# Kernel optimization log

Hardware: AMD Instinct MI355X
Metric: run time of the kernel (lower is better)

The kernel has to match this reference:

```python
import jax, jax.numpy as jnp
import numpy as np

EMBED_DIM = 1024
NUM_HEADS = 16
HEAD_DIM = EMBED_DIM // NUM_HEADS
SCALE = HEAD_DIM ** -0.5
EPS = 1e-5


def layer_norm(x, gamma, beta):
    mu = jnp.mean(x, axis=-1, keepdims=True)
    var = jnp.var(x, axis=-1, keepdims=True)
    return (x - mu) * jax.lax.rsqrt(var + EPS) * gamma + beta


def setup_inputs() -> dict:
    key = jax.random.key(0)
    ks = jax.random.split(key, 12)
    d = EMBED_DIM
    xav = (6.0 / (d + d)) ** 0.5
    x = jax.random.normal(ks[0], (4, 1024, d), dtype=jnp.float32)
    Wq = jax.random.uniform(ks[1], (d, d), jnp.float32, -xav, xav)
    Wk = jax.random.uniform(ks[2], (d, d), jnp.float32, -xav, xav)
    Wv = jax.random.uniform(ks[3], (d, d), jnp.float32, -xav, xav)
    Wo = jax.random.uniform(ks[4], (d, d), jnp.float32, -xav, xav)
    bq = jnp.zeros((d,), jnp.float32)
    bk = jnp.zeros((d,), jnp.float32)
    bv = jnp.zeros((d,), jnp.float32)
    bo = jnp.zeros((d,), jnp.float32)
    ones = jnp.ones((d,), jnp.float32)
    zeros = jnp.zeros((d,), jnp.float32)
    return {
        "x": x,
        "Wq": Wq, "bq": bq, "Wk": Wk, "bk": bk, "Wv": Wv, "bv": bv,
        "Wo": Wo, "bo": bo,
        "qn_g": ones, "qn_b": zeros,
        "kn_g": ones, "kn_b": zeros,
        "vn_g": ones, "vn_b": zeros,
        "on_g": ones, "on_b": zeros,
    }


def reference(x, Wq, bq, Wk, bk, Wv, bv, Wo, bo,
              qn_g, qn_b, kn_g, kn_b, vn_g, vn_b, on_g, on_b):
    B, S, D = x.shape
    H, Hd = NUM_HEADS, HEAD_DIM
    # projections (nn.Linear: x @ W.T + b) followed by LayerNorm
    Q = layer_norm(x @ Wq.T + bq, qn_g, qn_b) * SCALE
    K = layer_norm(x @ Wk.T + bk, kn_g, kn_b)
    V = layer_norm(x @ Wv.T + bv, vn_g, vn_b)
    Q = Q.reshape(B, S, H, Hd).transpose(0, 2, 1, 3)  # [B,H,S,Hd]
    K = K.reshape(B, S, H, Hd).transpose(0, 2, 1, 3)
    V = V.reshape(B, S, H, Hd).transpose(0, 2, 1, 3)
    scores = jnp.einsum('bhqd,bhkd->bhqk', Q, K)
    scores = jnp.clip(scores, -10.0, 10.0)
    attn = jax.nn.softmax(scores, axis=-1)  # dropout = identity at eval
    out = jnp.einsum('bhqk,bhkd->bhqd', attn, V)
    out = out.transpose(0, 2, 1, 3).reshape(B, S, D)
    out = out @ Wo.T + bo
    return layer_norm(out, on_g, on_b)
```

## Files before the change

kernel.cpp:

```cpp
#include <hip/hip_runtime.h>
#include <stdint.h>
#include <stddef.h>

typedef unsigned short u16;
typedef __bf16 bf16x8 __attribute__((ext_vector_type(8)));
typedef float f32x4 __attribute__((ext_vector_type(4)));
typedef u16 u16x8 __attribute__((ext_vector_type(8)));

#define SEQ    1024
#define DEMB   1024
#define MROWS  4096
#define NHEAD  16
#define HD     64
#define QSCALE 0.125f
#define LN_EPS 1e-5f

static __device__ __forceinline__ u16 f2bf(float f) {
  union { float f; unsigned u; } c; c.f = f;
  unsigned r = c.u + 0x7FFFu + ((c.u >> 16) & 1u);
  return (u16)(r >> 16);
}
static __device__ __forceinline__ float bf2f(unsigned h) {
  union { unsigned u; float f; } c; c.u = h << 16; return c.f;
}

static __device__ __forceinline__ void gload16(const void* g, void* l) {
  __builtin_amdgcn_global_load_lds((const __attribute__((address_space(1))) void*)g,
                                   (__attribute__((address_space(3))) void*)l, 16, 0, 0);
}

__global__ void cvt_kernel(const float* __restrict__ x,
                           const float* __restrict__ wq, const float* __restrict__ wk,
                           const float* __restrict__ wv, const float* __restrict__ wo,
                           u16* __restrict__ xb, u16* __restrict__ wb) {
  size_t e = ((size_t)blockIdx.x * blockDim.x + threadIdx.x) * 8;
  const float* src; u16* dst; size_t off;
  if (e < (size_t)MROWS * DEMB) { src = x; dst = xb; off = e; }
  else {
    size_t we = e - (size_t)MROWS * DEMB;
    int plane = (int)(we >> 20);
    src = (plane == 0) ? wq : (plane == 1) ? wk : (plane == 2) ? wv : wo;
    dst = wb + ((size_t)plane << 20);
    off = we & ((1u << 20) - 1);
  }
  float4 a = *(const float4*)(src + off);
  float4 b = *(const float4*)(src + off + 4);
  u16 o[8] = { f2bf(a.x), f2bf(a.y), f2bf(a.z), f2bf(a.w),
               f2bf(b.x), f2bf(b.y), f2bf(b.z), f2bf(b.w) };
  uint4 pk;
  pk.x = (unsigned)o[0] | ((unsigned)o[1] << 16);
  pk.y = (unsigned)o[2] | ((unsigned)o[3] << 16);
  pk.z = (unsigned)o[4] | ((unsigned)o[5] << 16);
  pk.w = (unsigned)o[6] | ((unsigned)o[7] << 16);
  *(uint4*)(dst + off) = pk;
}

__global__ __launch_bounds__(256)
void gemm_bt(const u16* __restrict__ A, const u16* __restrict__ B0,
             const u16* __restrict__ B1, const u16* __restrict__ B2,
             u16* __restrict__ C, int M, int N, int K) {
  __shared__ u16 lA[128 * 32];
  __shared__ u16 lB[128 * 32];
  const u16* Bp = (blockIdx.z == 0) ? B0 : (blockIdx.z == 1) ? B1 : B2;
  u16* Cp = C + (size_t)blockIdx.z * ((size_t)M * N);
  const int tid = threadIdx.x;
  const int w = tid >> 6, l = tid & 63;
  const int lr = l & 15, lg = l >> 4;
  const int m0 = blockIdx.x * 128, n0 = blockIdx.y * 128;
  const int wm = (w & 1) * 64, wn = (w >> 1) * 64;
  f32x4 acc[4][4] = {};
  const int cid0 = w * 64 + l;
  const int cid1 = 256 + w * 64 + l;
  const int rowA0 = cid0 >> 2, kc0 = (cid0 & 3) * 8;
  const int rowA1 = cid1 >> 2, kc1 = (cid1 & 3) * 8;
  for (int kt = 0; kt < K; kt += 32) {
    __syncthreads();
    gload16(A  + (size_t)(m0 + rowA0) * K + kt + kc0, lA + (size_t)(w * 64) * 8);
    gload16(A  + (size_t)(m0 + rowA1) * K + kt + kc1, lA + (size_t)(256 + w * 64) * 8);
    gload16(Bp + (size_t)(n0 + rowA0) * K + kt + kc0, lB + (size_t)(w * 64) * 8);
    gload16(Bp + (size_t)(n0 + rowA1) * K + kt + kc1, lB + (size_t)(256 + w * 64) * 8);
    __syncthreads();
    bf16x8 af[4], bfg[4];
#pragma unroll
    for (int mb = 0; mb < 4; ++mb)
      af[mb] = *(const bf16x8*)(lA + (wm + mb * 16 + lr) * 32 + lg * 8);
#pragma unroll
    for (int nb = 0; nb < 4; ++nb)
      bfg[nb] = *(const bf16x8*)(lB + (wn + nb * 16 + lr) * 32 + lg * 8);
#pragma unroll
    for (int mb = 0; mb < 4; ++mb)
#pragma unroll
      for (int nb = 0; nb < 4; ++nb)
        acc[mb][nb] = __builtin_amdgcn_mfma_f32_16x16x32_bf16(af[mb], bfg[nb], acc[mb][nb], 0, 0, 0);
  }
#pragma unroll
  for (int mb = 0; mb < 4; ++mb)
#pragma unroll
    for (int nb = 0; nb < 4; ++nb)
#pragma unroll
      for (int r = 0; r < 4; ++r) {
        int row = m0 + wm + mb * 16 + lg * 4 + r;
        int col = n0 + wn + nb * 16 + lr;
        Cp[(size_t)row * N + col] = f2bf(acc[mb][nb][r]);
      }
}

static __device__ __forceinline__ void block_reduce2(float& s1, float& s2, float* red) {
#pragma unroll
  for (int o = 32; o > 0; o >>= 1) { s1 += __shfl_xor(s1, o); s2 += __shfl_xor(s2, o); }
  int w = threadIdx.x >> 6, l = threadIdx.x & 63;
  if (l == 0) { red[w * 2] = s1; red[w * 2 + 1] = s2; }
  __syncthreads();
  s1 = red[0] + red[2] + red[4] + red[6];
  s2 = red[1] + red[3] + red[5] + red[7];
}

__global__ void ln_qkv_kernel(const u16* __restrict__ projb,
                              const float* __restrict__ bq, const float* __restrict__ bk,
                              const float* __restrict__ bv,
                              const float* __restrict__ qg, const float* __restrict__ qb,
                              const float* __restrict__ kg, const float* __restrict__ kb,
                              const float* __restrict__ vg, const float* __restrict__ vb,
                              u16* __restrict__ Qh, u16* __restrict__ Kh, u16* __restrict__ Vh) {
  __shared__ float red[8];
  const int row = blockIdx.x & (MROWS - 1);
  const int plane = blockIdx.x >> 12;
  const float* bias; const float* gam; const float* bet; u16* op; float scl;
  if (plane == 0)      { bias = bq; gam = qg; bet = qb; op = Qh; scl = QSCALE; }
  else if (plane == 1) { bias = bk; gam = kg; bet = kb; op = Kh; scl = 1.f; }
  else                 { bias = bv; gam = vg; bet = vb; op = Vh; scl = 1.f; }
  const u16* src = projb + ((size_t)plane * MROWS + row) * DEMB;
  const int t = threadIdx.x;
  uint2 pv = *(const uint2*)(src + t * 4);
  float4 v;
  v.x = bf2f(pv.x & 0xffffu); v.y = bf2f(pv.x >> 16);
  v.z = bf2f(pv.y & 0xffffu); v.w = bf2f(pv.y >> 16);
  float4 bz = *(const float4*)(bias + t * 4);
  v.x += bz.x; v.y += bz.y; v.z += bz.z; v.w += bz.w;
  float s1 = v.x + v.y + v.z + v.w;
  float s2 = v.x * v.x + v.y * v.y + v.z * v.z + v.w * v.w;
  block_reduce2(s1, s2, red);
  const float mean = s1 * (1.f / DEMB);
  const float var = s2 * (1.f / DEMB) - mean * mean;
  const float rstd = rsqrtf(var + LN_EPS);
  float4 gg = *(const float4*)(gam + t * 4);
  float4 bb = *(const float4*)(bet + t * 4);
  u16 o0 = f2bf(((v.x - mean) * rstd * gg.x + bb.x) * scl);
  u16 o1 = f2bf(((v.y - mean) * rstd * gg.y + bb.y) * scl);
  u16 o2 = f2bf(((v.z - mean) * rstd * gg.z + bb.z) * scl);
  u16 o3 = f2bf(((v.w - mean) * rstd * gg.w + bb.w) * scl);
  const int b = row >> 10, s = row & (SEQ - 1);
  const int h = t >> 4;
  u16* dst = op + ((size_t)(b * NHEAD + h) * SEQ + s) * HD + (t & 15) * 4;
  uint2 pk;
  pk.x = (unsigned)o0 | ((unsigned)o1 << 16);
  pk.y = (unsigned)o2 | ((unsigned)o3 << 16);
  *(uint2*)dst = pk;
}

__global__ __launch_bounds__(256)
void attn_kernel(const u16* __restrict__ Qh, const u16* __restrict__ Kh,
                 const u16* __restrict__ Vh, u16* __restrict__ AO) {
  __shared__ u16 Vt[64][72];
  __shared__ u16 Pt[4][16][72];
  const int qt = blockIdx.x & 15, bh = blockIdx.x >> 4;
  const int b = bh >> 4, h = bh & 15;
  const u16* Qp = Qh + (size_t)bh * SEQ * HD;
  const u16* Kp = Kh + (size_t)bh * SEQ * HD;
  const u16* Vp = Vh + (size_t)bh * SEQ * HD;
  const int tid = threadIdx.x, w = tid >> 6, l = tid & 63;
  const int lr = l & 15, lg = l >> 4;
  const int qrow = qt * 64 + w * 16 + lr;
  bf16x8 qa0 = *(const bf16x8*)(Qp + (size_t)qrow * HD + lg * 8);
  bf16x8 qa1 = *(const bf16x8*)(Qp + (size_t)qrow * HD + 32 + lg * 8);
  f32x4 o[4] = {};
  float rs[4] = {0.f, 0.f, 0.f, 0.f};
  for (int kt = 0; kt < SEQ / 64; ++kt) {
    __syncthreads();
#pragma unroll
    for (int i = 0; i < 2; ++i) {
      const int dc = w * 2 + i;
      u16x8 vv = *(const u16x8*)(Vp + (size_t)(kt * 64 + l) * HD + dc * 8);
#pragma unroll
      for (int ee = 0; ee < 8; ++ee) Vt[dc * 8 + ee][l] = vv[ee];
    }
#pragma unroll
    for (int kb = 0; kb < 4; ++kb) {
      const u16* kr = Kp + (size_t)(kt * 64 + kb * 16 + lr) * HD + lg * 8;
      bf16x8 k0 = *(const bf16x8*)kr;
      bf16x8 k1 = *(const bf16x8*)(kr + 32);
      f32x4 sv = {};
      sv = __builtin_amdgcn_mfma_f32_16x16x32_bf16(qa0, k0, sv, 0, 0, 0);
      sv = __builtin_amdgcn_mfma_f32_16x16x32_bf16(qa1, k1, sv, 0, 0, 0);
#pragma unroll
      for (int r = 0; r < 4; ++r) {
        float xx = fminf(10.f, fmaxf(-10.f, sv[r]));
        float p = exp2f(xx * 1.4426950408889634f);
        rs[r] += p;
        Pt[w][lg * 4 + r][kb * 16 + lr] = f2bf(p);
      }
    }
    __syncthreads();
    bf16x8 pa0 = *(const bf16x8*)(&Pt[w][lr][lg * 8]);
    bf16x8 pa1 = *(const bf16x8*)(&Pt[w][lr][32 + lg * 8]);
#pragma unroll
    for (int nb = 0; nb < 4; ++nb) {
      bf16x8 v0 = *(const bf16x8*)(&Vt[nb * 16 + lr][lg * 8]);
      bf16x8 v1 = *(const bf16x8*)(&Vt[nb * 16 + lr][32 + lg * 8]);
      o[nb] = __builtin_amdgcn_mfma_f32_16x16x32_bf16(pa0, v0, o[nb], 0, 0, 0);
      o[nb] = __builtin_amdgcn_mfma_f32_16x16x32_bf16(pa1, v1, o[nb], 0, 0, 0);
    }
  }
#pragma unroll
  for (int r = 0; r < 4; ++r) {
    float vsum = rs[r];
    vsum += __shfl_xor(vsum, 1);
    vsum += __shfl_xor(vsum, 2);
    vsum += __shfl_xor(vsum, 4);
    vsum += __shfl_xor(vsum, 8);
    rs[r] = vsum;
  }
#pragma unroll
  for (int nb = 0; nb < 4; ++nb)
#pragma unroll
    for (int r = 0; r < 4; ++r) {
      const int srow = qt * 64 + w * 16 + lg * 4 + r;
      const int col = h * HD + nb * 16 + lr;
      AO[((size_t)b * SEQ + srow) * DEMB + col] = f2bf(o[nb][r] / rs[r]);
    }
}

__global__ void ln_out_kernel(const u16* __restrict__ src0, const float* __restrict__ bo,
                              const float* __restrict__ og, const float* __restrict__ ob,
                              float* __restrict__ out) {
  __shared__ float red[8];
  const int row = blockIdx.x;
  const u16* src = src0 + (size_t)row * DEMB;
  const int t = threadIdx.x;
  uint2 pv = *(const uint2*)(src + t * 4);
  float4 v;
  v.x = bf2f(pv.x & 0xffffu); v.y = bf2f(pv.x >> 16);
  v.z = bf2f(pv.y & 0xffffu); v.w = bf2f(pv.y >> 16);
  float4 bz = *(const float4*)(bo + t * 4);
  v.x += bz.x; v.y += bz.y; v.z += bz.z; v.w += bz.w;
  float s1 = v.x + v.y + v.z + v.w;
  float s2 = v.x * v.x + v.y * v.y + v.z * v.z + v.w * v.w;
  block_reduce2(s1, s2, red);
  const float mean = s1 * (1.f / DEMB);
  const float var = s2 * (1.f / DEMB) - mean * mean;
  const float rstd = rsqrtf(var + LN_EPS);
  float4 gg = *(const float4*)(og + t * 4);
  float4 bb = *(const float4*)(ob + t * 4);
  float4 r;
  r.x = (v.x - mean) * rstd * gg.x + bb.x;
  r.y = (v.y - mean) * rstd * gg.y + bb.y;
  r.z = (v.z - mean) * rstd * gg.z + bb.z;
  r.w = (v.w - mean) * rstd * gg.w + bb.w;
  *(float4*)(out + (size_t)row * DEMB + t * 4) = r;
}

extern "C" void kernel_launch(void* const* d_in, const int* in_sizes, int n_in,
                              void* d_out, int out_size, void* d_ws, size_t ws_size,
                              hipStream_t stream) {
  (void)in_sizes; (void)n_in; (void)out_size; (void)ws_size;
  const float* x  = (const float*)d_in[0];
  const float* Wq = (const float*)d_in[1];
  const float* bq = (const float*)d_in[2];
  const float* Wk = (const float*)d_in[3];
  const float* bk = (const float*)d_in[4];
  const float* Wv = (const float*)d_in[5];
  const float* bv = (const float*)d_in[6];
  const float* Wo = (const float*)d_in[7];
  const float* bo = (const float*)d_in[8];
  const float* qg = (const float*)d_in[9];
  const float* qb = (const float*)d_in[10];
  const float* kg = (const float*)d_in[11];
  const float* kb = (const float*)d_in[12];
  const float* vg = (const float*)d_in[13];
  const float* vb = (const float*)d_in[14];
  const float* og = (const float*)d_in[15];
  const float* ob = (const float*)d_in[16];

  char* ws = (char*)d_ws;
  u16* xb    = (u16*)(ws);
  u16* wb    = (u16*)(ws + ((size_t)8  << 20));
  u16* projb = (u16*)(ws + ((size_t)16 << 20));
  u16* Qh    = (u16*)(ws + ((size_t)40 << 20));
  u16* Kh    = (u16*)(ws + ((size_t)48 << 20));
  u16* Vh    = (u16*)(ws + ((size_t)56 << 20));
  u16* AOp   = xb;
  u16* oprojb = projb;

  cvt_kernel<<<4096, 256, 0, stream>>>(x, Wq, Wk, Wv, Wo, xb, wb);

  dim3 gqkv(32, 8, 3);
  gemm_bt<<<gqkv, 256, 0, stream>>>(xb, wb, wb + (1u << 20), wb + (2u << 20),
                                    projb, MROWS, DEMB, DEMB);

  ln_qkv_kernel<<<3 * MROWS, 256, 0, stream>>>(projb, bq, bk, bv,
                                               qg, qb, kg, kb, vg, vb,
                                               Qh, Kh, Vh);

  attn_kernel<<<1024, 256, 0, stream>>>(Qh, Kh, Vh, AOp);

  dim3 go(32, 8, 1);
  gemm_bt<<<go, 256, 0, stream>>>(AOp, wb + (3u << 20), wb + (3u << 20), wb + (3u << 20),
                                  oprojb, MROWS, DEMB, DEMB);

  ln_out_kernel<<<MROWS, 256, 0, stream>>>(oprojb, bo, og, ob, (float*)d_out);
}
```

Baseline: 266.4 us.

## Pre-transpose V globally and restructure attention into single-wave 32-row blocks

Adds a separate kernel that writes V transposed per head to global memory, so the attention kernel can load V^T fragments straight from global instead of transposing into shared memory every key tile. The attention kernel becomes one wave per block handling 32 query rows (two MFMA row tiles that share K/V loads), which removes block-wide __syncthreads. The block index is also remapped to group work across heads. In exchange it adds an extra kernel launch with a round trip through memory, and the attention loop now reads K and V^T directly from global memory with no shared staging.

```diff
diff --git a/kernel.cpp b/kernel.cpp
--- a/kernel.cpp
+++ b/kernel.cpp
@@ -159,75 +159,116 @@
 }
 
 __global__ __launch_bounds__(256)
+void vtr_kernel(const u16* __restrict__ Vtmp, u16* __restrict__ VT) {
+  __shared__ u16 t[64][72];
+  const int stile = blockIdx.x & 15, bh = blockIdx.x >> 4;
+  const u16* src = Vtmp + ((size_t)bh * SEQ + stile * 64) * HD;
+  const int tid = threadIdx.x;
+  {
+    const int c0 = tid * 2;
+    const int r = c0 >> 3, c = c0 & 7;
+    uint4 v0 = *(const uint4*)(src + (size_t)r * HD + c * 8);
+    uint4 v1 = *(const uint4*)(src + (size_t)r * HD + (c + 1) * 8);
+    *(uint4*)&t[r][c * 8] = v0;
+    *(uint4*)&t[r][(c + 1) * 8] = v1;
+  }
+  __syncthreads();
+  const int d = tid >> 2, sc = tid & 3;
+  u16 buf[16];
+#pragma unroll
+  for (int j = 0; j < 16; ++j) buf[j] = t[sc * 16 + j][d];
+  u16* dst = VT + ((size_t)bh * HD + d) * SEQ + stile * 64 + sc * 16;
+  *(uint4*)(dst)     = *(uint4*)&buf[0];
+  *(uint4*)(dst + 8) = *(uint4*)&buf[8];
+}
+
+__global__ __launch_bounds__(64)
 void attn_kernel(const u16* __restrict__ Qh, const u16* __restrict__ Kh,
-                 const u16* __restrict__ Vh, u16* __restrict__ AO) {
-  __shared__ u16 Vt[64][72];
-  __shared__ u16 Pt[4][16][72];
-  const int qt = blockIdx.x & 15, bh = blockIdx.x >> 4;
+                 const u16* __restrict__ VT, u16* __restrict__ AO) {
+  __shared__ u16 Pt[32][76];
+  const int bid = blockIdx.x;
+  const int wg = (bid & 7) * 256 + (bid >> 3);
+  const int qt = wg & 31, bh = wg >> 5;
   const int b = bh >> 4, h = bh & 15;
   const u16* Qp = Qh + (size_t)bh * SEQ * HD;
   const u16* Kp = Kh + (size_t)bh * SEQ * HD;
-  const u16* Vp = Vh + (size_t)bh * SEQ * HD;
-  const int tid = threadIdx.x, w = tid >> 6, l = tid & 63;
+  const u16* Vp = VT + (size_t)bh * HD * SEQ;
+  const int l = threadIdx.x;
   const int lr = l & 15, lg = l >> 4;
-  const int qrow = qt * 64 + w * 16 + lr;
-  bf16x8 qa0 = *(const bf16x8*)(Qp + (size_t)qrow * HD + lg * 8);
-  bf16x8 qa1 = *(const bf16x8*)(Qp + (size_t)qrow * HD + 32 + lg * 8);
-  f32x4 o[4] = {};
-  float rs[4] = {0.f, 0.f, 0.f, 0.f};
+  bf16x8 qa[2][2];
+#pragma unroll
+  for (int m = 0; m < 2; ++m) {
+    const u16* qr = Qp + (size_t)(qt * 32 + m * 16 + lr) * HD + lg * 8;
+    qa[m][0] = *(const bf16x8*)qr;
+    qa[m][1] = *(const bf16x8*)(qr + 32);
+  }
+  f32x4 o[2][4] = {};
+  float rs[2][4] = {{0.f,0.f,0.f,0.f},{0.f,0.f,0.f,0.f}};
   for (int kt = 0; kt < SEQ / 64; ++kt) {
-    __syncthreads();
-#pragma unroll
-    for (int i = 0; i < 2; ++i) {
-      const int dc = w * 2 + i;
-      u16x8 vv = *(const u16x8*)(Vp + (size_t)(kt * 64 + l) * HD + dc * 8);
-#pragma unroll
-      for (int ee = 0; ee < 8; ++ee) Vt[dc * 8 + ee][l] = vv[ee];
-    }
+    f32x4 sv[2][4];
 #pragma unroll
     for (int kb = 0; kb < 4; ++kb) {
       const u16* kr = Kp + (size_t)(kt * 64 + kb * 16 + lr) * HD + lg * 8;
       bf16x8 k0 = *(const bf16x8*)kr;
       bf16x8 k1 = *(const bf16x8*)(kr + 32);
-      f32x4 sv = {};
-      sv = __builtin_amdgcn_mfma_f32_16x16x32_bf16(qa0, k0, sv, 0, 0, 0);
-      sv = __builtin_amdgcn_mfma_f32_16x16x32_bf16(qa1, k1, sv, 0, 0, 0);
-#pragma unroll
-      for (int r = 0; r < 4; ++r) {
-        float xx = fminf(10.f, fmaxf(-10.f, sv[r]));
-        float p = exp2f(xx * 1.4426950408889634f);
-        rs[r] += p;
-        Pt[w][lg * 4 + r][kb * 16 + lr] = f2bf(p);
+#pragma unroll
+      for (int m = 0; m < 2; ++m) {
+        f32x4 s0 = {};
+        s0 = __builtin_amdgcn_mfma_f32_16x16x32_bf16(qa[m][0], k0, s0, 0, 0, 0);
+        s0 = __builtin_amdgcn_mfma_f32_16x16x32_bf16(qa[m][1], k1, s0, 0, 0, 0);
+        sv[m][kb] = s0;
       }
     }
-    __syncthreads();
-    bf16x8 pa0 = *(const bf16x8*)(&Pt[w][lr][lg * 8]);
-    bf16x8 pa1 = *(const bf16x8*)(&Pt[w][lr][32 + lg * 8]);
+#pragma unroll
+    for (int m = 0; m < 2; ++m)
+#pragma unroll
+      for (int kb = 0; kb < 4; ++kb)
+#pragma unroll
+        for (int r = 0; r < 4; ++r) {
+          float xx = fminf(10.f, fmaxf(-10.f, sv[m][kb][r]));
+          float p = exp2f(xx * 1.4426950408889634f);
+          rs[m][r] += p;
+          Pt[m * 16 + lg * 4 + r][kb * 16 + lr] = f2bf(p);
+        }
+    bf16x8 pa[2][2];
+#pragma unroll
+    for (int m = 0; m < 2; ++m) {
+      pa[m][0] = *(const bf16x8*)&Pt[m * 16 + lr][lg * 8];
+      pa[m][1] = *(const bf16x8*)&Pt[m * 16 + lr][32 + lg * 8];
+    }
 #pragma unroll
     for (int nb = 0; nb < 4; ++nb) {
-      bf16x8 v0 = *(const bf16x8*)(&Vt[nb * 16 + lr][lg * 8]);
-      bf16x8 v1 = *(const bf16x8*)(&Vt[nb * 16 + lr][32 + lg * 8]);
-      o[nb] = __builtin_amdgcn_mfma_f32_16x16x32_bf16(pa0, v0, o[nb], 0, 0, 0);
-      o[nb] = __builtin_amdgcn_mfma_f32_16x16x32_bf16(pa1, v1, o[nb], 0, 0, 0);
+      const u16* vr = Vp + (size_t)(nb * 16 + lr) * SEQ + kt * 64 + lg * 8;
+      bf16x8 v0 = *(const bf16x8*)vr;
+      bf16x8 v1 = *(const bf16x8*)(vr + 32);
+#pragma unroll
+      for (int m = 0; m < 2; ++m) {
+        o[m][nb] = __builtin_amdgcn_mfma_f32_16x16x32_bf16(pa[m][0], v0, o[m][nb], 0, 0, 0);
+        o[m][nb] = __builtin_amdgcn_mfma_f32_16x16x32_bf16(pa[m][1], v1, o[m][nb], 0, 0, 0);
+      }
     }
   }
 #pragma unroll
-  for (int r = 0; r < 4; ++r) {
-    float vsum = rs[r];
-    vsum += __shfl_xor(vsum, 1);
-    vsum += __shfl_xor(vsum, 2);
-    vsum += __shfl_xor(vsum, 4);
-    vsum += __shfl_xor(vsum, 8);
-    rs[r] = vsum;
-  }
-#pragma unroll
-  for (int nb = 0; nb < 4; ++nb)
+  for (int m = 0; m < 2; ++m)
 #pragma unroll
     for (int r = 0; r < 4; ++r) {
-      const int srow = qt * 64 + w * 16 + lg * 4 + r;
-      const int col = h * HD + nb * 16 + lr;
-      AO[((size_t)b * SEQ + srow) * DEMB + col] = f2bf(o[nb][r] / rs[r]);
+      float vsum = rs[m][r];
+      vsum += __shfl_xor(vsum, 1);
+      vsum += __shfl_xor(vsum, 2);
+      vsum += __shfl_xor(vsum, 4);
+      vsum += __shfl_xor(vsum, 8);
+      rs[m][r] = vsum;
     }
+#pragma unroll
+  for (int m = 0; m < 2; ++m)
+#pragma unroll
+    for (int nb = 0; nb < 4; ++nb)
+#pragma unroll
+      for (int r = 0; r < 4; ++r) {
+        const int srow = qt * 32 + m * 16 + lg * 4 + r;
+        const int col = h * HD + nb * 16 + lr;
+        AO[((size_t)b * SEQ + srow) * DEMB + col] = f2bf(o[m][nb][r] / rs[m][r]);
+      }
 }
 
 __global__ void ln_out_kernel(const u16* __restrict__ src0, const float* __restrict__ bo,
@@ -287,7 +328,8 @@
   u16* projb = (u16*)(ws + ((size_t)16 << 20));
   u16* Qh    = (u16*)(ws + ((size_t)40 << 20));
   u16* Kh    = (u16*)(ws + ((size_t)48 << 20));
-  u16* Vh    = (u16*)(ws + ((size_t)56 << 20));
+  u16* VT    = (u16*)(ws + ((size_t)56 << 20));
+  u16* Vtmp  = xb;
   u16* AOp   = xb;
   u16* oprojb = projb;
 
@@ -299,9 +341,11 @@
 
   ln_qkv_kernel<<<3 * MROWS, 256, 0, stream>>>(projb, bq, bk, bv,
                                                qg, qb, kg, kb, vg, vb,
-                                               Qh, Kh, Vh);
-
-  attn_kernel<<<1024, 256, 0, stream>>>(Qh, Kh, Vh, AOp);
+                                               Qh, Kh, Vtmp);
+
+  vtr_kernel<<<1024, 256, 0, stream>>>(Vtmp, VT);
+
+  attn_kernel<<<2048, 64, 0, stream>>>(Qh, Kh, VT, AOp);
 
   dim3 go(32, 8, 1);
   gemm_bt<<<go, 256, 0, stream>>>(AOp, wb + (3u << 20), wb + (3u << 20), wb + (3u << 20),
```

Result: no change. 262.1 us (-1.6%).
